# Optimization experiments

Measured on AMD Instinct MI355X. Metric: run time of the kernel, lower is better.

The kernel has to match this reference:

```python
import jax, jax.numpy as jnp
import numpy as np

N_NODES = 50000
N_EDGES = 150000
D_FEAT = 512
HIDDEN = 512
N_CLASSES = 47


def gcn_conv(x, edge_index, W, b, n_nodes):
    """PyG GCNConv: out = D^{-1/2} (A + I) D^{-1/2} (x @ W) + b."""
    h = x @ W  # [N, out_dim] dense GEMM
    loop = jnp.arange(n_nodes, dtype=edge_index.dtype)
    row = jnp.concatenate([edge_index[0], loop])  # source
    col = jnp.concatenate([edge_index[1], loop])  # target
    ones = jnp.ones(row.shape[0], dtype=h.dtype)
    deg = jax.ops.segment_sum(ones, col, num_segments=n_nodes)  # in-degree + 1
    dinv = jnp.where(deg > 0, jax.lax.rsqrt(deg), 0.0)
    norm = dinv[row] * dinv[col]  # [E+N]
    msg = norm[:, None] * h[row]  # gather + scale
    out = jax.ops.segment_sum(msg, col, num_segments=n_nodes)  # scatter-add
    return out + b


def setup_inputs() -> dict:
    key = jax.random.key(0)
    k1, k2, k3, k4, k5, k6 = jax.random.split(key, 6)
    x = jax.random.normal(k1, (N_NODES, D_FEAT), dtype=jnp.float32)
    edge_index = jax.random.randint(k2, (2, N_EDGES), 0, N_NODES, dtype=jnp.int64)
    s1 = (6.0 / (D_FEAT + HIDDEN)) ** 0.5
    s2 = (6.0 / (HIDDEN + N_CLASSES)) ** 0.5
    W1 = jax.random.uniform(k3, (D_FEAT, HIDDEN), jnp.float32, -s1, s1)
    b1 = jnp.zeros((HIDDEN,), jnp.float32)
    W2 = jax.random.uniform(k4, (HIDDEN, N_CLASSES), jnp.float32, -s2, s2)
    b2 = jnp.zeros((N_CLASSES,), jnp.float32)
    return {"x": x, "edge_index": edge_index, "W1": W1, "b1": b1, "W2": W2, "b2": b2}


def reference(x, edge_index, W1, b1, W2, b2):
    n = x.shape[0]
    h = gcn_conv(x, edge_index, W1, b1, n)
    h = jax.nn.relu(h)
    # F.dropout(p=0.5, training=self.training): eval mode -> identity
    out = gcn_conv(h, edge_index, W2, b2, n)
    return out
```

## Files before the change

kernel.cpp:

```cpp
#include <hip/hip_runtime.h>
#include <hip/hip_bf16.h>

#define NNODES 50000
#define NEDGES 150000
#define DFEAT  512
#define HID    512
#define NCLS   47

typedef __hip_bfloat16 bf16;
typedef __attribute__((ext_vector_type(8))) short short8;
typedef __attribute__((ext_vector_type(4))) float float4v;

typedef const __attribute__((address_space(1))) unsigned int* gas_t;
typedef __attribute__((address_space(3))) unsigned int* las_t;
__device__ __forceinline__ void load_lds16(const void* g, void* l) {
    __builtin_amdgcn_global_load_lds((gas_t)g, (las_t)l, 16, 0, 0);
}

__device__ __forceinline__ float bfbits_lo(unsigned int w) {
    return __uint_as_float((w & 0xFFFFu) << 16);
}
__device__ __forceinline__ float bfbits_hi(unsigned int w) {
    return __uint_as_float(w & 0xFFFF0000u);
}

__global__ void k_detect(const void* x, const void* ei, int* flags) {
    __shared__ int scnt[64], sor[64];
    int t = threadIdx.x;
    const unsigned short* xs = (const unsigned short*)x;
    int c = 0;
    for (int i = t; i < 256; i += 64) {
        unsigned int e = (xs[2 * i] >> 7) & 0xFF;
        c += (e >= 117 && e <= 130) ? 1 : 0;
    }
    const int* w = (const int*)ei;
    int o = 0;
    for (int i = 2 * t + 1; i < 512; i += 128) o |= w[i];
    scnt[t] = c; sor[t] = o;
    __syncthreads();
    if (t == 0) {
        int C = 0, O = 0;
        for (int i = 0; i < 64; i++) { C += scnt[i]; O |= sor[i]; }
        flags[0] = (C > 128) ? 1 : 0;
        flags[1] = (O == 0) ? 1 : 0;
    }
}

__device__ __forceinline__ int eidx(const void* ei, int half, int e, int is64) {
    if (is64) return (int)((const long long*)ei)[(size_t)half * NEDGES + e];
    return ((const int*)ei)[half * NEDGES + e];
}

__global__ void k_zero32(unsigned int* p, size_t n) {
    size_t i = (size_t)blockIdx.x * blockDim.x + threadIdx.x;
    if (i < n) p[i] = 0u;
}

__global__ void k_cvt(const void* src, float* dst, int n, const int* flags) {
    int i = blockIdx.x * blockDim.x + threadIdx.x;
    if (i >= n) return;
    dst[i] = flags[0] ? __bfloat162float(((const bf16*)src)[i]) : ((const float*)src)[i];
}

__global__ void k_cvt_w1t(const void* W1, bf16* W1T, const int* flags) {
    int i = blockIdx.x * blockDim.x + threadIdx.x;
    if (i >= DFEAT * HID) return;
    int k = i / HID, n = i % HID;
    float v = flags[0] ? __bfloat162float(((const bf16*)W1)[i]) : ((const float*)W1)[i];
    W1T[(size_t)n * DFEAT + k] = __float2bfloat16(v);
}

__global__ void k_cvt_w2t(const void* W2, bf16* W2T, const int* flags) {
    int i = blockIdx.x * blockDim.x + threadIdx.x;
    if (i >= 64 * HID) return;
    int n = i / HID, k = i % HID;
    float v = 0.0f;
    if (n < NCLS) {
        size_t idx = (size_t)k * NCLS + n;
        v = flags[0] ? __bfloat162float(((const bf16*)W2)[idx]) : ((const float*)W2)[idx];
    }
    W2T[(size_t)n * HID + k] = __float2bfloat16(v);
}

__global__ void k_count(const void* ei, int* cnt, const int* flags) {
    int e = blockIdx.x * blockDim.x + threadIdx.x;
    if (e >= NEDGES) return;
    atomicAdd(&cnt[eidx(ei, 1, e, flags[1])], 1);
}

__global__ void k_dinv(const int* cnt, float* dinv) {
    int i = blockIdx.x * blockDim.x + threadIdx.x;
    if (i < NNODES) dinv[i] = rsqrtf(1.0f + (float)cnt[i]);
}

__global__ __launch_bounds__(256) void k_scan_part(const int* cnt, int* part) {
    __shared__ int s[256];
    int i = blockIdx.x * 256 + threadIdx.x;
    s[threadIdx.x] = (i < NNODES) ? cnt[i] : 0;
    __syncthreads();
    for (int off = 128; off > 0; off >>= 1) {
        if (threadIdx.x < off) s[threadIdx.x] += s[threadIdx.x + off];
        __syncthreads();
    }
    if (threadIdx.x == 0) part[blockIdx.x] = s[0];
}

__global__ __launch_bounds__(256) void k_scan_off(int* part, int n) {
    __shared__ int s[256];
    int v = (threadIdx.x < n) ? part[threadIdx.x] : 0;
    s[threadIdx.x] = v;
    __syncthreads();
    for (int off = 1; off < 256; off <<= 1) {
        int t = (threadIdx.x >= off) ? s[threadIdx.x - off] : 0;
        __syncthreads();
        s[threadIdx.x] += t;
        __syncthreads();
    }
    if (threadIdx.x < n) part[threadIdx.x] = s[threadIdx.x] - v;
}

__global__ __launch_bounds__(256) void k_scan_fin(const int* cnt, const int* part,
                                                  int* rowptr, int* cursor) {
    __shared__ int s[256];
    int i = blockIdx.x * 256 + threadIdx.x;
    int v = (i < NNODES) ? cnt[i] : 0;
    s[threadIdx.x] = v;
    __syncthreads();
    for (int off = 1; off < 256; off <<= 1) {
        int t = (threadIdx.x >= off) ? s[threadIdx.x - off] : 0;
        __syncthreads();
        s[threadIdx.x] += t;
        __syncthreads();
    }
    int incl = s[threadIdx.x] + part[blockIdx.x];
    if (i < NNODES) {
        rowptr[i + 1] = incl;
        cursor[i] = incl - v;
    }
    if (i == 0) rowptr[0] = 0;
}

__global__ void k_fill(const void* ei, int* cursor, int* csr_src, const int* flags) {
    int e = blockIdx.x * blockDim.x + threadIdx.x;
    if (e >= NEDGES) return;
    int is64 = flags[1];
    int v = eidx(ei, 1, e, is64);
    int u = eidx(ei, 0, e, is64);
    int pos = atomicAdd(&cursor[v], 1);
    csr_src[pos] = u;
}

__global__ __launch_bounds__(256, 3) void k_gemm1_v3(
    const void* __restrict__ X, const bf16* __restrict__ W1T,
    bf16* __restrict__ h1c, int c0, int C, const int* __restrict__ flags,
    int col_tiles, int rows_per_xcd, int n_row_tiles) {
    const int b = blockIdx.x;
    const int xcd = b & 7;
    const int s = b >> 3;
    const int col_t = s % col_tiles;
    const int lr = s / col_tiles;
    const int row_t = xcd * rows_per_xcd + lr;
    if (row_t >= n_row_tiles) return;

    __shared__ bf16 As[128 * 64];
    __shared__ bf16 Bs[128 * 64];
    const int tid = threadIdx.x;
    const int wave = tid >> 6, lane = tid & 63;
    const int row0 = row_t * 128;
    const int gc0 = c0 + col_t * 128;
    const int isb = flags[0];

    float4v acc[2][8];
#pragma unroll
    for (int i = 0; i < 2; i++)
#pragma unroll
        for (int j = 0; j < 8; j++) acc[i][j] = (float4v){0.f, 0.f, 0.f, 0.f};

    const int rb = wave * 32;
    const int frow = lane & 15;
    const int fk = lane >> 4;

    for (int k0 = 0; k0 < DFEAT; k0 += 64) {
        __syncthreads();
        if (isb) {
            const bf16* xb = (const bf16*)X;
#pragma unroll
            for (int t = 0; t < 4; ++t) {
                int g8 = wave * 4 + t;
                int r = g8 * 8 + (lane >> 3);
                int gr = row0 + r; if (gr >= NNODES) gr = NNODES - 1;
                int ck = (lane & 7) ^ (r & 7);
                load_lds16(xb + (size_t)gr * DFEAT + k0 + ck * 8, &As[g8 * 8 * 64]);
            }
        } else {
            const float* xf = (const float*)X;
            for (int i = tid; i < 128 * 8; i += 256) {
                int r = i >> 3, p = i & 7;
                int gr = row0 + r; if (gr >= NNODES) gr = NNODES - 1;
                int ck = p ^ (r & 7);
                const float* src = xf + (size_t)gr * DFEAT + k0 + ck * 8;
#pragma unroll
                for (int e = 0; e < 8; ++e)
                    As[r * 64 + p * 8 + e] = __float2bfloat16(src[e]);
            }
        }
#pragma unroll
        for (int t = 0; t < 4; ++t) {
            int g8 = wave * 4 + t;
            int cl = g8 * 8 + (lane >> 3);
            int ck = (lane & 7) ^ (cl & 7);
            load_lds16(W1T + (size_t)(gc0 + cl) * DFEAT + k0 + ck * 8, &Bs[g8 * 8 * 64]);
        }
        __syncthreads();
#pragma unroll
        for (int ki = 0; ki < 2; ++ki) {
            const int cc = ki * 4 + fk;
            short8 a[2], b8[8];
#pragma unroll
            for (int i = 0; i < 2; i++) {
                int r = rb + i * 16 + frow;
                a[i] = *(const short8*)&As[r * 64 + (cc ^ (r & 7)) * 8];
            }
#pragma unroll
            for (int j = 0; j < 8; j++) {
                int cl = j * 16 + frow;
                b8[j] = *(const short8*)&Bs[cl * 64 + (cc ^ (cl & 7)) * 8];
            }
#pragma unroll
            for (int i = 0; i < 2; i++)
#pragma unroll
                for (int j = 0; j < 8; j++)
                    acc[i][j] = __builtin_amdgcn_mfma_f32_16x16x32_bf16(a[i], b8[j], acc[i][j], 0, 0, 0);
        }
    }
    const int ccol = gc0 - c0;
#pragma unroll
    for (int i = 0; i < 2; i++) {
#pragma unroll
        for (int r = 0; r < 4; r++) {
            int grow = row0 + rb + i * 16 + (lane >> 4) * 4 + r;
            if (grow < NNODES) {
#pragma unroll
                for (int j = 0; j < 8; j++)
                    h1c[(size_t)grow * C + ccol + j * 16 + (lane & 15)] =
                        __float2bfloat16(acc[i][j][r]);
            }
        }
    }
}

__global__ __launch_bounds__(256) void k_gemm1_mfma(
    const void* __restrict__ X, const bf16* __restrict__ W1T,
    bf16* __restrict__ h1c, int c0, int C, const int* __restrict__ flags) {
    __shared__ bf16 As[128 * 64];
    __shared__ bf16 Bs[64 * 64];
    const int tid = threadIdx.x;
    const int wave = tid >> 6, lane = tid & 63;
    const int row0 = blockIdx.x * 128;
    const int gc0 = c0 + blockIdx.y * 64;
    const int isb = flags[0];
    float4v acc[2][4];
#pragma unroll
    for (int i = 0; i < 2; i++)
#pragma unroll
        for (int j = 0; j < 4; j++) acc[i][j] = (float4v){0.f, 0.f, 0.f, 0.f};
    const int rbase = wave * 32;
    const int fl_row = lane & 15;
    const int fl_k8 = (lane >> 4) * 8;
    for (int k0 = 0; k0 < DFEAT; k0 += 64) {
        __syncthreads();
        if (isb) {
            const bf16* xb = (const bf16*)X;
#pragma unroll
            for (int i = 0; i < 4; ++i) {
                int r = i * 32 + wave * 8;
                int gr = row0 + r + (lane >> 3);
                if (gr >= NNODES) gr = NNODES - 1;
                load_lds16(xb + (size_t)gr * DFEAT + k0 + (lane & 7) * 8, &As[r * 64]);
            }
        } else {
            const float* xf = (const float*)X;
            for (int i = tid; i < 128 * 64; i += 256) {
                int r = i >> 6, c = i & 63;
                int gr = row0 + r;
                if (gr >= NNODES) gr = NNODES - 1;
                As[i] = __float2bfloat16(xf[(size_t)gr * DFEAT + k0 + c]);
            }
        }
#pragma unroll
        for (int i = 0; i < 2; ++i) {
            int r = i * 32 + wave * 8;
            int gn = gc0 + r + (lane >> 3);
            load_lds16(W1T + (size_t)gn * DFEAT + k0 + (lane & 7) * 8, &Bs[r * 64]);
        }
        __syncthreads();
#pragma unroll
        for (int ki = 0; ki < 64; ki += 32) {
            short8 a[2], b[4];
#pragma unroll
            for (int i = 0; i < 2; i++)
                a[i] = *(const short8*)&As[(rbase + i * 16 + fl_row) * 64 + ki + fl_k8];
#pragma unroll
            for (int j = 0; j < 4; j++)
                b[j] = *(const short8*)&Bs[(j * 16 + fl_row) * 64 + ki + fl_k8];
#pragma unroll
            for (int i = 0; i < 2; i++)
#pragma unroll
                for (int j = 0; j < 4; j++)
                    acc[i][j] = __builtin_amdgcn_mfma_f32_16x16x32_bf16(a[i], b[j], acc[i][j], 0, 0, 0);
        }
    }
    const int ccol = blockIdx.y * 64;
#pragma unroll
    for (int i = 0; i < 2; i++) {
#pragma unroll
        for (int r = 0; r < 4; r++) {
            int grow = row0 + rbase + i * 16 + (lane >> 4) * 4 + r;
            if (grow < NNODES) {
#pragma unroll
                for (int j = 0; j < 4; j++)
                    h1c[(size_t)grow * C + ccol + j * 16 + (lane & 15)] =
                        __float2bfloat16(acc[i][j][r]);
            }
        }
    }
}

__global__ __launch_bounds__(256) void k_agg1_512(const bf16* __restrict__ h1c,
                                                  const int* __restrict__ rowptr,
                                                  const int* __restrict__ csr_src,
                                                  const float* __restrict__ dinv,
                                                  const float* __restrict__ b1c,
                                                  bf16* __restrict__ a1c) {
    int v = blockIdx.x * 4 + (threadIdx.x >> 6);
    int lane = threadIdx.x & 63;
    if (v >= NNODES) return;
    int d8 = lane * 8;
    float dv = dinv[v];
    float s2 = dv * dv;
    uint4 w = *(const uint4*)(h1c + (size_t)v * 512 + d8);
    float a0 = s2 * bfbits_lo(w.x), a1 = s2 * bfbits_hi(w.x);
    float a2 = s2 * bfbits_lo(w.y), a3 = s2 * bfbits_hi(w.y);
    float a4 = s2 * bfbits_lo(w.z), a5 = s2 * bfbits_hi(w.z);
    float a6 = s2 * bfbits_lo(w.w), a7 = s2 * bfbits_hi(w.w);
    int pend = rowptr[v + 1];
    for (int p = rowptr[v]; p < pend; ++p) {
        int u = csr_src[p];
        float nw = dinv[u] * dv;
        uint4 q = *(const uint4*)(h1c + (size_t)u * 512 + d8);
        a0 += nw * bfbits_lo(q.x); a1 += nw * bfbits_hi(q.x);
        a2 += nw * bfbits_lo(q.y); a3 += nw * bfbits_hi(q.y);
        a4 += nw * bfbits_lo(q.z); a5 += nw * bfbits_hi(q.z);
        a6 += nw * bfbits_lo(q.w); a7 += nw * bfbits_hi(q.w);
    }
    const float* bb = b1c + d8;
    a0 += bb[0]; a1 += bb[1]; a2 += bb[2]; a3 += bb[3];
    a4 += bb[4]; a5 += bb[5]; a6 += bb[6]; a7 += bb[7];
    bf16 o[8];
    o[0] = __float2bfloat16(a0 > 0.f ? a0 : 0.f);
    o[1] = __float2bfloat16(a1 > 0.f ? a1 : 0.f);
    o[2] = __float2bfloat16(a2 > 0.f ? a2 : 0.f);
    o[3] = __float2bfloat16(a3 > 0.f ? a3 : 0.f);
    o[4] = __float2bfloat16(a4 > 0.f ? a4 : 0.f);
    o[5] = __float2bfloat16(a5 > 0.f ? a5 : 0.f);
    o[6] = __float2bfloat16(a6 > 0.f ? a6 : 0.f);
    o[7] = __float2bfloat16(a7 > 0.f ? a7 : 0.f);
    *(uint4*)(a1c + (size_t)v * 512 + d8) = *(uint4*)o;
}

__global__ __launch_bounds__(256) void k_agg1(const bf16* __restrict__ h1c,
                                              const int* __restrict__ rowptr,
                                              const int* __restrict__ csr_src,
                                              const float* __restrict__ dinv,
                                              const float* __restrict__ b1c, int c0, int C,
                                              bf16* __restrict__ a1c) {
    const int tshift = (C == 512) ? 7 : (C == 256) ? 6 : (C == 128) ? 5 : 4;
    long long gt = (long long)blockIdx.x * 256 + threadIdx.x;
    int v = (int)(gt >> tshift);
    int d4 = (int)((gt & ((1 << tshift) - 1)) << 2);
    if (v >= NNODES) return;
    float dv = dinv[v];
    uint2 w = *(const uint2*)(h1c + (size_t)v * C + d4);
    float s2 = dv * dv;
    float a0 = s2 * bfbits_lo(w.x), a1 = s2 * bfbits_hi(w.x);
    float a2 = s2 * bfbits_lo(w.y), a3 = s2 * bfbits_hi(w.y);
    int pend = rowptr[v + 1];
    for (int p = rowptr[v]; p < pend; ++p) {
        int u = csr_src[p];
        float nw = dinv[u] * dv;
        uint2 q = *(const uint2*)(h1c + (size_t)u * C + d4);
        a0 += nw * bfbits_lo(q.x); a1 += nw * bfbits_hi(q.x);
        a2 += nw * bfbits_lo(q.y); a3 += nw * bfbits_hi(q.y);
    }
    const float* bb = b1c + c0 + d4;
    a0 += bb[0]; a1 += bb[1]; a2 += bb[2]; a3 += bb[3];
    bf16 o[4];
    o[0] = __float2bfloat16(a0 > 0.f ? a0 : 0.f);
    o[1] = __float2bfloat16(a1 > 0.f ? a1 : 0.f);
    o[2] = __float2bfloat16(a2 > 0.f ? a2 : 0.f);
    o[3] = __float2bfloat16(a3 > 0.f ? a3 : 0.f);
    *(uint2*)(a1c + (size_t)v * C + d4) = *(uint2*)o;
}

__global__ __launch_bounds__(256) void k_gemm2_mfma(
    const bf16* __restrict__ A, int C, const bf16* __restrict__ W2T, int kg0,
    float* __restrict__ h2, int accum) {
    __shared__ bf16 As[128 * 64];
    __shared__ bf16 Bs[64 * 64];
    const int tid = threadIdx.x;
    const int wave = tid >> 6, lane = tid & 63;
    const int row0 = blockIdx.x * 128;
    float4v acc[2][4];
#pragma unroll
    for (int i = 0; i < 2; i++)
#pragma unroll
        for (int j = 0; j < 4; j++) acc[i][j] = (float4v){0.f, 0.f, 0.f, 0.f};
    const int rbase = wave * 32;
    const int fl_row = lane & 15;
    const int fl_k8 = (lane >> 4) * 8;
    for (int kk = 0; kk < C; kk += 64) {
        __syncthreads();
#pragma unroll
        for (int i = 0; i < 4; ++i) {
            int r = i * 32 + wave * 8;
            int gr = row0 + r + (lane >> 3);
            if (gr >= NNODES) gr = NNODES - 1;
            load_lds16(A + (size_t)gr * C + kk + (lane & 7) * 8, &As[r * 64]);
        }
#pragma unroll
        for (int i = 0; i < 2; ++i) {
            int r = i * 32 + wave * 8;
            int gn = r + (lane >> 3);
            load_lds16(W2T + (size_t)gn * HID + kg0 + kk + (lane & 7) * 8, &Bs[r * 64]);
        }
        __syncthreads();
#pragma unroll
        for (int ki = 0; ki < 64; ki += 32) {
            short8 a[2], b[4];
#pragma unroll
            for (int i = 0; i < 2; i++)
                a[i] = *(const short8*)&As[(rbase + i * 16 + fl_row) * 64 + ki + fl_k8];
#pragma unroll
            for (int j = 0; j < 4; j++)
                b[j] = *(const short8*)&Bs[(j * 16 + fl_row) * 64 + ki + fl_k8];
#pragma unroll
            for (int i = 0; i < 2; i++)
#pragma unroll
                for (int j = 0; j < 4; j++)
                    acc[i][j] = __builtin_amdgcn_mfma_f32_16x16x32_bf16(a[i], b[j], acc[i][j], 0, 0, 0);
        }
    }
#pragma unroll
    for (int i = 0; i < 2; i++) {
#pragma unroll
        for (int r = 0; r < 4; r++) {
            int grow = row0 + rbase + i * 16 + (lane >> 4) * 4 + r;
            if (grow < NNODES) {
#pragma unroll
                for (int j = 0; j < 4; j++) {
                    int col = j * 16 + (lane & 15);
                    if (col < NCLS) {
                        size_t o = (size_t)grow * NCLS + col;
                        h2[o] = accum ? h2[o] + acc[i][j][r] : acc[i][j][r];
                    }
                }
            }
        }
    }
}

__global__ __launch_bounds__(256) void k_agg2(const float* __restrict__ h2,
                                              const int* __restrict__ rowptr,
                                              const int* __restrict__ csr_src,
                                              const float* __restrict__ dinv,
                                              const float* __restrict__ b2c,
                                              void* out, const int* flags) {
    int v = blockIdx.x * 4 + (threadIdx.x >> 6);
    int d = threadIdx.x & 63;
    if (v >= NNODES || d >= NCLS) return;
    float dv = dinv[v];
    float acc = dv * dv * h2[(size_t)v * NCLS + d];
    int pend = rowptr[v + 1];
    for (int p = rowptr[v]; p < pend; ++p) {
        int u = csr_src[p];
        acc += dinv[u] * dv * h2[(size_t)u * NCLS + d];
    }
    acc += b2c[d];
    size_t o = (size_t)v * NCLS + d;
    if (flags[0]) ((bf16*)out)[o] = __float2bfloat16(acc);
    else          ((float*)out)[o] = acc;
}

extern "C" void kernel_launch(void* const* d_in, const int* in_sizes, int n_in,
                              void* d_out, int out_size, void* d_ws, size_t ws_size,
                              hipStream_t stream) {
    const void* x  = d_in[0];
    const void* ei = d_in[1];
    const void* W1 = d_in[2];
    const void* b1 = d_in[3];
    const void* W2 = d_in[4];
    const void* b2 = d_in[5];

    char* base = (char*)d_ws;
    auto alloc = [&](size_t bytes) -> char* {
        char* p = base;
        base += (bytes + 255) & ~(size_t)255;
        return p;
    };
    int*   flags  = (int*)alloc(64);
    int*   cnt    = (int*)alloc(sizeof(int) * NNODES);
    int*   part   = (int*)alloc(sizeof(int) * 256);
    int*   rowptr = (int*)alloc(sizeof(int) * (NNODES + 1));
    int*   cursor = (int*)alloc(sizeof(int) * NNODES);
    int*   csr    = (int*)alloc(sizeof(int) * NEDGES);
    float* dinv   = (float*)alloc(sizeof(float) * NNODES);
    bf16*  W1T    = (bf16*)alloc(sizeof(bf16) * DFEAT * HID);
    float* b1c    = (float*)alloc(sizeof(float) * HID);
    bf16*  W2T    = (bf16*)alloc(sizeof(bf16) * 64 * HID);
    float* b2c    = (float*)alloc(sizeof(float) * 64);
    float* h2     = (float*)alloc(sizeof(float) * (size_t)NNODES * NCLS);

    size_t used = (size_t)(base - (char*)d_ws);
    size_t rem = (ws_size > used) ? ws_size - used : 0;
    int C = 64;
    if (rem >= (size_t)200000 * 512 + 1024) C = 512;
    else if (rem >= (size_t)200000 * 256 + 1024) C = 256;
    else if (rem >= (size_t)200000 * 128 + 1024) C = 128;
    bf16* h1c = (bf16*)alloc(sizeof(bf16) * (size_t)NNODES * C);
    bf16* a1c = (bf16*)alloc(sizeof(bf16) * (size_t)NNODES * C);

    k_detect<<<1, 64, 0, stream>>>(x, ei, flags);
    k_zero32<<<(NNODES + 255) / 256, 256, 0, stream>>>((unsigned int*)cnt, NNODES);

    k_cvt_w1t<<<(DFEAT * HID + 255) / 256, 256, 0, stream>>>(W1, W1T, flags);
    k_cvt<<<(HID + 255) / 256, 256, 0, stream>>>(b1, b1c, HID, flags);
    k_cvt_w2t<<<(64 * HID + 255) / 256, 256, 0, stream>>>(W2, W2T, flags);
    k_cvt<<<1, 64, 0, stream>>>(b2, b2c, NCLS, flags);

    k_count<<<(NEDGES + 255) / 256, 256, 0, stream>>>(ei, cnt, flags);
    k_dinv<<<(NNODES + 255) / 256, 256, 0, stream>>>(cnt, dinv);
    const int nsb = (NNODES + 255) / 256;
    k_scan_part<<<nsb, 256, 0, stream>>>(cnt, part);
    k_scan_off<<<1, 256, 0, stream>>>(part, nsb);
    k_scan_fin<<<nsb, 256, 0, stream>>>(cnt, part, rowptr, cursor);
    k_fill<<<(NEDGES + 255) / 256, 256, 0, stream>>>(ei, cursor, csr, flags);

    const int rowblocks = (NNODES + 127) / 128;
    const int rows_per_xcd = (rowblocks + 7) / 8;
    int chunk_i = 0;
    for (int c0 = 0; c0 < HID; c0 += C, ++chunk_i) {
        if (C >= 128) {
            int col_tiles = C / 128;
            int nblk = 8 * rows_per_xcd * col_tiles;
            k_gemm1_v3<<<nblk, 256, 0, stream>>>(x, W1T, h1c, c0, C, flags,
                                                 col_tiles, rows_per_xcd, rowblocks);
        } else {
            dim3 g1(rowblocks, 1);
            k_gemm1_mfma<<<g1, 256, 0, stream>>>(x, W1T, h1c, c0, C, flags);
        }
        if (C == 512) {
            k_agg1_512<<<(NNODES + 3) / 4, 256, 0, stream>>>(h1c, rowptr, csr, dinv, b1c, a1c);
        } else {
            size_t nthr = (size_t)NNODES * (C / 4);
            k_agg1<<<(int)((nthr + 255) / 256), 256, 0, stream>>>(h1c, rowptr, csr, dinv, b1c, c0, C, a1c);
        }
        k_gemm2_mfma<<<rowblocks, 256, 0, stream>>>(a1c, C, W2T, c0, h2, chunk_i > 0 ? 1 : 0);
    }

    k_agg2<<<(NNODES + 3) / 4, 256, 0, stream>>>(h2, rowptr, csr, dinv, b2c, d_out, flags);
}
```

Measured before the change: 348.9 us.

## Double-buffer LDS tiles in both GEMM kernels and swizzle gemm2 layout

```diff
diff --git a/kernel.cpp b/kernel.cpp
--- a/kernel.cpp
+++ b/kernel.cpp
@@ -150,7 +150,7 @@
     csr_src[pos] = u;
 }
 
-__global__ __launch_bounds__(256, 3) void k_gemm1_v3(
+__global__ __launch_bounds__(256, 2) void k_gemm1_v4(
     const void* __restrict__ X, const bf16* __restrict__ W1T,
     bf16* __restrict__ h1c, int c0, int C, const int* __restrict__ flags,
     int col_tiles, int rows_per_xcd, int n_row_tiles) {
@@ -162,8 +162,8 @@
     const int row_t = xcd * rows_per_xcd + lr;
     if (row_t >= n_row_tiles) return;
 
-    __shared__ bf16 As[128 * 64];
-    __shared__ bf16 Bs[128 * 64];
+    __shared__ bf16 As[2][128 * 64];
+    __shared__ bf16 Bs[2][128 * 64];
     const int tid = threadIdx.x;
     const int wave = tid >> 6, lane = tid & 63;
     const int row0 = row_t * 128;
@@ -180,8 +180,7 @@
     const int frow = lane & 15;
     const int fk = lane >> 4;
 
-    for (int k0 = 0; k0 < DFEAT; k0 += 64) {
-        __syncthreads();
+    auto stageAB = [&](int k0, bf16* Asb, bf16* Bsb) {
         if (isb) {
             const bf16* xb = (const bf16*)X;
 #pragma unroll
@@ -190,7 +189,7 @@
                 int r = g8 * 8 + (lane >> 3);
                 int gr = row0 + r; if (gr >= NNODES) gr = NNODES - 1;
                 int ck = (lane & 7) ^ (r & 7);
-                load_lds16(xb + (size_t)gr * DFEAT + k0 + ck * 8, &As[g8 * 8 * 64]);
+                load_lds16(xb + (size_t)gr * DFEAT + k0 + ck * 8, Asb + g8 * 8 * 64);
             }
         } else {
             const float* xf = (const float*)X;
@@ -201,7 +200,7 @@
                 const float* src = xf + (size_t)gr * DFEAT + k0 + ck * 8;
 #pragma unroll
                 for (int e = 0; e < 8; ++e)
-                    As[r * 64 + p * 8 + e] = __float2bfloat16(src[e]);
+                    Asb[r * 64 + p * 8 + e] = __float2bfloat16(src[e]);
             }
         }
 #pragma unroll
@@ -209,9 +208,18 @@
             int g8 = wave * 4 + t;
             int cl = g8 * 8 + (lane >> 3);
             int ck = (lane & 7) ^ (cl & 7);
-            load_lds16(W1T + (size_t)(gc0 + cl) * DFEAT + k0 + ck * 8, &Bs[g8 * 8 * 64]);
-        }
-        __syncthreads();
+            load_lds16(W1T + (size_t)(gc0 + cl) * DFEAT + k0 + ck * 8, Bsb + g8 * 8 * 64);
+        }
+    };
+
+    stageAB(0, As[0], Bs[0]);
+    __syncthreads();
+    int cur = 0;
+
+    for (int k0 = 0; k0 < DFEAT; k0 += 64) {
+        if (k0 + 64 < DFEAT) stageAB(k0 + 64, As[cur ^ 1], Bs[cur ^ 1]);
+        const bf16* Ac = As[cur];
+        const bf16* Bc = Bs[cur];
 #pragma unroll
         for (int ki = 0; ki < 2; ++ki) {
             const int cc = ki * 4 + fk;
@@ -219,12 +227,12 @@
 #pragma unroll
             for (int i = 0; i < 2; i++) {
                 int r = rb + i * 16 + frow;
-                a[i] = *(const short8*)&As[r * 64 + (cc ^ (r & 7)) * 8];
+                a[i] = *(const short8*)&Ac[r * 64 + (cc ^ (r & 7)) * 8];
             }
 #pragma unroll
             for (int j = 0; j < 8; j++) {
                 int cl = j * 16 + frow;
-                b8[j] = *(const short8*)&Bs[cl * 64 + (cc ^ (cl & 7)) * 8];
+                b8[j] = *(const short8*)&Bc[cl * 64 + (cc ^ (cl & 7)) * 8];
             }
 #pragma unroll
             for (int i = 0; i < 2; i++)
@@ -232,7 +240,10 @@
                 for (int j = 0; j < 8; j++)
                     acc[i][j] = __builtin_amdgcn_mfma_f32_16x16x32_bf16(a[i], b8[j], acc[i][j], 0, 0, 0);
         }
-    }
+        __syncthreads();
+        cur ^= 1;
+    }
+
     const int ccol = gc0 - c0;
 #pragma unroll
     for (int i = 0; i < 2; i++) {
@@ -402,11 +413,11 @@
     *(uint2*)(a1c + (size_t)v * C + d4) = *(uint2*)o;
 }
 
-__global__ __launch_bounds__(256) void k_gemm2_mfma(
+__global__ __launch_bounds__(256, 3) void k_gemm2_v2(
     const bf16* __restrict__ A, int C, const bf16* __restrict__ W2T, int kg0,
     float* __restrict__ h2, int accum) {
-    __shared__ bf16 As[128 * 64];
-    __shared__ bf16 Bs[64 * 64];
+    __shared__ bf16 As[2][128 * 64];
+    __shared__ bf16 Bs[2][64 * 64];
     const int tid = threadIdx.x;
     const int wave = tid >> 6, lane = tid & 63;
     const int row0 = blockIdx.x * 128;
@@ -415,46 +426,64 @@
     for (int i = 0; i < 2; i++)
 #pragma unroll
         for (int j = 0; j < 4; j++) acc[i][j] = (float4v){0.f, 0.f, 0.f, 0.f};
-    const int rbase = wave * 32;
-    const int fl_row = lane & 15;
-    const int fl_k8 = (lane >> 4) * 8;
+    const int rb = wave * 32;
+    const int frow = lane & 15;
+    const int fk = lane >> 4;
+
+    auto stage2 = [&](int kk, bf16* Asb, bf16* Bsb) {
+#pragma unroll
+        for (int t = 0; t < 4; ++t) {
+            int g8 = wave * 4 + t;
+            int r = g8 * 8 + (lane >> 3);
+            int gr = row0 + r; if (gr >= NNODES) gr = NNODES - 1;
+            int ck = (lane & 7) ^ (r & 7);
+            load_lds16(A + (size_t)gr * C + kk + ck * 8, Asb + g8 * 8 * 64);
+        }
+#pragma unroll
+        for (int t = 0; t < 2; ++t) {
+            int g8 = wave * 2 + t;
+            int cl = g8 * 8 + (lane >> 3);
+            int ck = (lane & 7) ^ (cl & 7);
+            load_lds16(W2T + (size_t)cl * HID + kg0 + kk + ck * 8, Bsb + g8 * 8 * 64);
+        }
+    };
+
+    stage2(0, As[0], Bs[0]);
+    __syncthreads();
+    int cur = 0;
+
     for (int kk = 0; kk < C; kk += 64) {
-        __syncthreads();
-#pragma unroll
-        for (int i = 0; i < 4; ++i) {
-            int r = i * 32 + wave * 8;
-            int gr = row0 + r + (lane >> 3);
-            if (gr >= NNODES) gr = NNODES - 1;
-            load_lds16(A + (size_t)gr * C + kk + (lane & 7) * 8, &As[r * 64]);
-        }
-#pragma unroll
-        for (int i = 0; i < 2; ++i) {
-            int r = i * 32 + wave * 8;
-            int gn = r + (lane >> 3);
-            load_lds16(W2T + (size_t)gn * HID + kg0 + kk + (lane & 7) * 8, &Bs[r * 64]);
-        }
-        __syncthreads();
-#pragma unroll
-        for (int ki = 0; ki < 64; ki += 32) {
-            short8 a[2], b[4];
+        if (kk + 64 < C) stage2(kk + 64, As[cur ^ 1], Bs[cur ^ 1]);
+        const bf16* Ac = As[cur];
+        const bf16* Bc = Bs[cur];
+#pragma unroll
+        for (int ki = 0; ki < 2; ++ki) {
+            const int cc = ki * 4 + fk;
+            short8 a[2], b8[4];
+#pragma unroll
+            for (int i = 0; i < 2; i++) {
+                int r = rb + i * 16 + frow;
+                a[i] = *(const short8*)&Ac[r * 64 + (cc ^ (r & 7)) * 8];
+            }
+#pragma unroll
+            for (int j = 0; j < 4; j++) {
+                int cl = j * 16 + frow;
+                b8[j] = *(const short8*)&Bc[cl * 64 + (cc ^ (cl & 7)) * 8];
+            }
 #pragma unroll
             for (int i = 0; i < 2; i++)
-                a[i] = *(const short8*)&As[(rbase + i * 16 + fl_row) * 64 + ki + fl_k8];
-#pragma unroll
-            for (int j = 0; j < 4; j++)
-                b[j] = *(const short8*)&Bs[(j * 16 + fl_row) * 64 + ki + fl_k8];
-#pragma unroll
-            for (int i = 0; i < 2; i++)
 #pragma unroll
                 for (int j = 0; j < 4; j++)
-                    acc[i][j] = __builtin_amdgcn_mfma_f32_16x16x32_bf16(a[i], b[j], acc[i][j], 0, 0, 0);
-        }
+                    acc[i][j] = __builtin_amdgcn_mfma_f32_16x16x32_bf16(a[i], b8[j], acc[i][j], 0, 0, 0);
+        }
+        __syncthreads();
+        cur ^= 1;
     }
 #pragma unroll
     for (int i = 0; i < 2; i++) {
 #pragma unroll
         for (int r = 0; r < 4; r++) {
-            int grow = row0 + rbase + i * 16 + (lane >> 4) * 4 + r;
+            int grow = row0 + rb + i * 16 + (lane >> 4) * 4 + r;
             if (grow < NNODES) {
 #pragma unroll
                 for (int j = 0; j < 4; j++) {
@@ -552,7 +581,7 @@
         if (C >= 128) {
             int col_tiles = C / 128;
             int nblk = 8 * rows_per_xcd * col_tiles;
-            k_gemm1_v3<<<nblk, 256, 0, stream>>>(x, W1T, h1c, c0, C, flags,
+            k_gemm1_v4<<<nblk, 256, 0, stream>>>(x, W1T, h1c, c0, C, flags,
                                                  col_tiles, rows_per_xcd, rowblocks);
         } else {
             dim3 g1(rowblocks, 1);
@@ -564,7 +593,7 @@
             size_t nthr = (size_t)NNODES * (C / 4);
             k_agg1<<<(int)((nthr + 255) / 256), 256, 0, stream>>>(h1c, rowptr, csr, dinv, b1c, c0, C, a1c);
         }
-        k_gemm2_mfma<<<rowblocks, 256, 0, stream>>>(a1c, C, W2T, c0, h2, chunk_i > 0 ? 1 : 0);
+        k_gemm2_v2<<<rowblocks, 256, 0, stream>>>(a1c, C, W2T, c0, h2, chunk_i > 0 ? 1 : 0);
     }
 
     k_agg2<<<(NNODES + 3) / 4, 256, 0, stream>>>(h2, rowptr, csr, dinv, b2c, d_out, flags);
```

Measured after the change: 370.8 us. 1.06x slower.

## Load MFMA fragments directly from global memory, dropping LDS staging in both GEMMs

Applied to the files above, without the earlier changes.

```diff
diff --git a/kernel.cpp b/kernel.cpp
--- a/kernel.cpp
+++ b/kernel.cpp
@@ -150,7 +150,23 @@
     csr_src[pos] = u;
 }
 
-__global__ __launch_bounds__(256, 3) void k_gemm1_v3(
+__device__ __forceinline__ short8 afrag_bf(const bf16* X, int row, int k) {
+    return *(const short8*)(X + (size_t)row * DFEAT + k);
+}
+__device__ __forceinline__ short8 afrag_f32(const float* X, int row, int k) {
+    const float* p = X + (size_t)row * DFEAT + k;
+    float4v f0 = *(const float4v*)p;
+    float4v f1 = *(const float4v*)(p + 4);
+    short8 r;
+    bf16* rb = (bf16*)&r;
+    rb[0] = __float2bfloat16(f0[0]); rb[1] = __float2bfloat16(f0[1]);
+    rb[2] = __float2bfloat16(f0[2]); rb[3] = __float2bfloat16(f0[3]);
+    rb[4] = __float2bfloat16(f1[0]); rb[5] = __float2bfloat16(f1[1]);
+    rb[6] = __float2bfloat16(f1[2]); rb[7] = __float2bfloat16(f1[3]);
+    return r;
+}
+
+__global__ __launch_bounds__(256, 3) void k_gemm1_v6(
     const void* __restrict__ X, const bf16* __restrict__ W1T,
     bf16* __restrict__ h1c, int c0, int C, const int* __restrict__ flags,
     int col_tiles, int rows_per_xcd, int n_row_tiles) {
@@ -162,77 +178,66 @@
     const int row_t = xcd * rows_per_xcd + lr;
     if (row_t >= n_row_tiles) return;
 
-    __shared__ bf16 As[128 * 64];
-    __shared__ bf16 Bs[128 * 64];
     const int tid = threadIdx.x;
     const int wave = tid >> 6, lane = tid & 63;
     const int row0 = row_t * 128;
     const int gc0 = c0 + col_t * 128;
     const int isb = flags[0];
 
-    float4v acc[2][8];
-#pragma unroll
-    for (int i = 0; i < 2; i++)
-#pragma unroll
-        for (int j = 0; j < 8; j++) acc[i][j] = (float4v){0.f, 0.f, 0.f, 0.f};
-
     const int rb = wave * 32;
     const int frow = lane & 15;
-    const int fk = lane >> 4;
-
-    for (int k0 = 0; k0 < DFEAT; k0 += 64) {
-        __syncthreads();
-        if (isb) {
-            const bf16* xb = (const bf16*)X;
-#pragma unroll
-            for (int t = 0; t < 4; ++t) {
-                int g8 = wave * 4 + t;
-                int r = g8 * 8 + (lane >> 3);
-                int gr = row0 + r; if (gr >= NNODES) gr = NNODES - 1;
-                int ck = (lane & 7) ^ (r & 7);
-                load_lds16(xb + (size_t)gr * DFEAT + k0 + ck * 8, &As[g8 * 8 * 64]);
-            }
-        } else {
-            const float* xf = (const float*)X;
-            for (int i = tid; i < 128 * 8; i += 256) {
-                int r = i >> 3, p = i & 7;
-                int gr = row0 + r; if (gr >= NNODES) gr = NNODES - 1;
-                int ck = p ^ (r & 7);
-                const float* src = xf + (size_t)gr * DFEAT + k0 + ck * 8;
-#pragma unroll
-                for (int e = 0; e < 8; ++e)
-                    As[r * 64 + p * 8 + e] = __float2bfloat16(src[e]);
-            }
-        }
-#pragma unroll
-        for (int t = 0; t < 4; ++t) {
-            int g8 = wave * 4 + t;
-            int cl = g8 * 8 + (lane >> 3);
-            int ck = (lane & 7) ^ (cl & 7);
-            load_lds16(W1T + (size_t)(gc0 + cl) * DFEAT + k0 + ck * 8, &Bs[g8 * 8 * 64]);
-        }
-        __syncthreads();
-#pragma unroll
-        for (int ki = 0; ki < 2; ++ki) {
-            const int cc = ki * 4 + fk;
+    const int fko = (lane >> 4) * 8;
+
+    int ar[2];
+#pragma unroll
+    for (int i = 0; i < 2; i++) {
+        int gr = row0 + rb + i * 16 + frow;
+        ar[i] = (gr >= NNODES) ? NNODES - 1 : gr;
+    }
+
+    float4v acc[2][8];
+#pragma unroll
+    for (int i = 0; i < 2; i++)
+#pragma unroll
+        for (int j = 0; j < 8; j++) acc[i][j] = (float4v){0.f, 0.f, 0.f, 0.f};
+
+    const bf16* xb = (const bf16*)X;
+    const float* xf = (const float*)X;
+
+    if (isb) {
+#pragma unroll 4
+        for (int k0 = 0; k0 < DFEAT; k0 += 32) {
+            const int kk = k0 + fko;
             short8 a[2], b8[8];
 #pragma unroll
-            for (int i = 0; i < 2; i++) {
-                int r = rb + i * 16 + frow;
-                a[i] = *(const short8*)&As[r * 64 + (cc ^ (r & 7)) * 8];
-            }
-#pragma unroll
-            for (int j = 0; j < 8; j++) {
-                int cl = j * 16 + frow;
-                b8[j] = *(const short8*)&Bs[cl * 64 + (cc ^ (cl & 7)) * 8];
-            }
+            for (int i = 0; i < 2; i++) a[i] = afrag_bf(xb, ar[i], kk);
+#pragma unroll
+            for (int j = 0; j < 8; j++)
+                b8[j] = *(const short8*)(W1T + (size_t)(gc0 + j * 16 + frow) * DFEAT + kk);
 #pragma unroll
             for (int i = 0; i < 2; i++)
 #pragma unroll
                 for (int j = 0; j < 8; j++)
                     acc[i][j] = __builtin_amdgcn_mfma_f32_16x16x32_bf16(a[i], b8[j], acc[i][j], 0, 0, 0);
         }
-    }
+    } else {
+#pragma unroll 2
+        for (int k0 = 0; k0 < DFEAT; k0 += 32) {
+            const int kk = k0 + fko;
+            short8 a[2], b8[8];
+#pragma unroll
+            for (int i = 0; i < 2; i++) a[i] = afrag_f32(xf, ar[i], kk);
+#pragma unroll
+            for (int j = 0; j < 8; j++)
+                b8[j] = *(const short8*)(W1T + (size_t)(gc0 + j * 16 + frow) * DFEAT + kk);
+#pragma unroll
+            for (int i = 0; i < 2; i++)
+#pragma unroll
+                for (int j = 0; j < 8; j++)
+                    acc[i][j] = __builtin_amdgcn_mfma_f32_16x16x32_bf16(a[i], b8[j], acc[i][j], 0, 0, 0);
+        }
+    }
+
     const int ccol = gc0 - c0;
 #pragma unroll
     for (int i = 0; i < 2; i++) {
@@ -242,7 +247,7 @@
             if (grow < NNODES) {
 #pragma unroll
                 for (int j = 0; j < 8; j++)
-                    h1c[(size_t)grow * C + ccol + j * 16 + (lane & 15)] =
+                    h1c[(size_t)grow * C + ccol + j * 16 + frow] =
                         __float2bfloat16(acc[i][j][r]);
             }
         }
@@ -402,63 +407,55 @@
     *(uint2*)(a1c + (size_t)v * C + d4) = *(uint2*)o;
 }
 
-__global__ __launch_bounds__(256) void k_gemm2_mfma(
+__global__ __launch_bounds__(256, 4) void k_gemm2_v4(
     const bf16* __restrict__ A, int C, const bf16* __restrict__ W2T, int kg0,
     float* __restrict__ h2, int accum) {
-    __shared__ bf16 As[128 * 64];
-    __shared__ bf16 Bs[64 * 64];
     const int tid = threadIdx.x;
     const int wave = tid >> 6, lane = tid & 63;
     const int row0 = blockIdx.x * 128;
+    const int rb = wave * 32;
+    const int frow = lane & 15;
+    const int fko = (lane >> 4) * 8;
+
+    int ar[2];
+#pragma unroll
+    for (int i = 0; i < 2; i++) {
+        int gr = row0 + rb + i * 16 + frow;
+        ar[i] = (gr >= NNODES) ? NNODES - 1 : gr;
+    }
+
     float4v acc[2][4];
 #pragma unroll
     for (int i = 0; i < 2; i++)
 #pragma unroll
         for (int j = 0; j < 4; j++) acc[i][j] = (float4v){0.f, 0.f, 0.f, 0.f};
-    const int rbase = wave * 32;
-    const int fl_row = lane & 15;
-    const int fl_k8 = (lane >> 4) * 8;
-    for (int kk = 0; kk < C; kk += 64) {
-        __syncthreads();
-#pragma unroll
-        for (int i = 0; i < 4; ++i) {
-            int r = i * 32 + wave * 8;
-            int gr = row0 + r + (lane >> 3);
-            if (gr >= NNODES) gr = NNODES - 1;
-            load_lds16(A + (size_t)gr * C + kk + (lane & 7) * 8, &As[r * 64]);
-        }
-#pragma unroll
-        for (int i = 0; i < 2; ++i) {
-            int r = i * 32 + wave * 8;
-            int gn = r + (lane >> 3);
-            load_lds16(W2T + (size_t)gn * HID + kg0 + kk + (lane & 7) * 8, &Bs[r * 64]);
-        }
-        __syncthreads();
-#pragma unroll
-        for (int ki = 0; ki < 64; ki += 32) {
-            short8 a[2], b[4];
-#pragma unroll
-            for (int i = 0; i < 2; i++)
-                a[i] = *(const short8*)&As[(rbase + i * 16 + fl_row) * 64 + ki + fl_k8];
+
+#pragma unroll 4
+    for (int k0 = 0; k0 < C; k0 += 32) {
+        const int kk = k0 + fko;
+        short8 a[2], b4[4];
+#pragma unroll
+        for (int i = 0; i < 2; i++)
+            a[i] = *(const short8*)(A + (size_t)ar[i] * C + kk);
+#pragma unroll
+        for (int j = 0; j < 4; j++)
+            b4[j] = *(const short8*)(W2T + (size_t)(j * 16 + frow) * HID + kg0 + kk);
+#pragma unroll
+        for (int i = 0; i < 2; i++)
 #pragma unroll
             for (int j = 0; j < 4; j++)
-                b[j] = *(const short8*)&Bs[(j * 16 + fl_row) * 64 + ki + fl_k8];
-#pragma unroll
-            for (int i = 0; i < 2; i++)
-#pragma unroll
-                for (int j = 0; j < 4; j++)
-                    acc[i][j] = __builtin_amdgcn_mfma_f32_16x16x32_bf16(a[i], b[j], acc[i][j], 0, 0, 0);
-        }
-    }
+                acc[i][j] = __builtin_amdgcn_mfma_f32_16x16x32_bf16(a[i], b4[j], acc[i][j], 0, 0, 0);
+    }
+
 #pragma unroll
     for (int i = 0; i < 2; i++) {
 #pragma unroll
         for (int r = 0; r < 4; r++) {
-            int grow = row0 + rbase + i * 16 + (lane >> 4) * 4 + r;
+            int grow = row0 + rb + i * 16 + (lane >> 4) * 4 + r;
             if (grow < NNODES) {
 #pragma unroll
                 for (int j = 0; j < 4; j++) {
-                    int col = j * 16 + (lane & 15);
+                    int col = j * 16 + frow;
                     if (col < NCLS) {
                         size_t o = (size_t)grow * NCLS + col;
                         h2[o] = accum ? h2[o] + acc[i][j][r] : acc[i][j][r];
@@ -552,7 +549,7 @@
         if (C >= 128) {
             int col_tiles = C / 128;
             int nblk = 8 * rows_per_xcd * col_tiles;
-            k_gemm1_v3<<<nblk, 256, 0, stream>>>(x, W1T, h1c, c0, C, flags,
+            k_gemm1_v6<<<nblk, 256, 0, stream>>>(x, W1T, h1c, c0, C, flags,
                                                  col_tiles, rows_per_xcd, rowblocks);
         } else {
             dim3 g1(rowblocks, 1);
@@ -564,7 +561,7 @@
             size_t nthr = (size_t)NNODES * (C / 4);
             k_agg1<<<(int)((nthr + 255) / 256), 256, 0, stream>>>(h1c, rowptr, csr, dinv, b1c, c0, C, a1c);
         }
-        k_gemm2_mfma<<<rowblocks, 256, 0, stream>>>(a1c, C, W2T, c0, h2, chunk_i > 0 ? 1 : 0);
+        k_gemm2_v4<<<rowblocks, 256, 0, stream>>>(a1c, C, W2T, c0, h2, chunk_i > 0 ? 1 : 0);
     }
 
     k_agg2<<<(NNODES + 3) / 4, 256, 0, stream>>>(h2, rowptr, csr, dinv, b2c, d_out, flags);
```

Result: slower. 424.7 us (+21.7%).

## Fuse prep kernels, merge dinv into scan, retile gemm2 with swizzled LDS

Applied to the files above, without the earlier changes.

```diff
diff --git a/kernel.cpp b/kernel.cpp
--- a/kernel.cpp
+++ b/kernel.cpp
@@ -24,62 +24,86 @@
     return __uint_as_float(w & 0xFFFF0000u);
 }
 
-__global__ void k_detect(const void* x, const void* ei, int* flags) {
-    __shared__ int scnt[64], sor[64];
-    int t = threadIdx.x;
-    const unsigned short* xs = (const unsigned short*)x;
-    int c = 0;
-    for (int i = t; i < 256; i += 64) {
-        unsigned int e = (xs[2 * i] >> 7) & 0xFF;
-        c += (e >= 117 && e <= 130) ? 1 : 0;
-    }
-    const int* w = (const int*)ei;
-    int o = 0;
-    for (int i = 2 * t + 1; i < 512; i += 128) o |= w[i];
-    scnt[t] = c; sor[t] = o;
-    __syncthreads();
-    if (t == 0) {
-        int C = 0, O = 0;
-        for (int i = 0; i < 64; i++) { C += scnt[i]; O |= sor[i]; }
-        flags[0] = (C > 128) ? 1 : 0;
-        flags[1] = (O == 0) ? 1 : 0;
-    }
-}
-
 __device__ __forceinline__ int eidx(const void* ei, int half, int e, int is64) {
     if (is64) return (int)((const long long*)ei)[(size_t)half * NEDGES + e];
     return ((const int*)ei)[half * NEDGES + e];
 }
 
-__global__ void k_zero32(unsigned int* p, size_t n) {
-    size_t i = (size_t)blockIdx.x * blockDim.x + threadIdx.x;
-    if (i < n) p[i] = 0u;
-}
-
-__global__ void k_cvt(const void* src, float* dst, int n, const int* flags) {
-    int i = blockIdx.x * blockDim.x + threadIdx.x;
-    if (i >= n) return;
-    dst[i] = flags[0] ? __bfloat162float(((const bf16*)src)[i]) : ((const float*)src)[i];
-}
-
-__global__ void k_cvt_w1t(const void* W1, bf16* W1T, const int* flags) {
-    int i = blockIdx.x * blockDim.x + threadIdx.x;
-    if (i >= DFEAT * HID) return;
-    int k = i / HID, n = i % HID;
-    float v = flags[0] ? __bfloat162float(((const bf16*)W1)[i]) : ((const float*)W1)[i];
-    W1T[(size_t)n * DFEAT + k] = __float2bfloat16(v);
-}
-
-__global__ void k_cvt_w2t(const void* W2, bf16* W2T, const int* flags) {
-    int i = blockIdx.x * blockDim.x + threadIdx.x;
-    if (i >= 64 * HID) return;
-    int n = i / HID, k = i % HID;
-    float v = 0.0f;
-    if (n < NCLS) {
-        size_t idx = (size_t)k * NCLS + n;
-        v = flags[0] ? __bfloat162float(((const bf16*)W2)[idx]) : ((const float*)W2)[idx];
-    }
-    W2T[(size_t)n * HID + k] = __float2bfloat16(v);
+#define ZB ((NNODES + 255) / 256)
+#define PR_W1T (1 + ZB)
+#define PR_B1  (PR_W1T + 1024)
+#define PR_W2T (PR_B1 + 2)
+#define PR_B2  (PR_W2T + 128)
+#define PR_GRID (PR_B2 + 1)
+
+__global__ __launch_bounds__(256) void k_prep0(
+    const void* x, const void* ei, const void* W1, const void* b1,
+    const void* W2, const void* b2, int* flags, unsigned int* cnt,
+    bf16* W1T, float* b1c, bf16* W2T, float* b2c) {
+    __shared__ int sh[128];
+    __shared__ int shflag;
+    const int b = blockIdx.x, t = threadIdx.x;
+
+    if (b >= 1 && b < 1 + ZB) {
+        int i = (b - 1) * 256 + t;
+        if (i < NNODES) cnt[i] = 0u;
+        return;
+    }
+
+    if (t < 64) {
+        const unsigned short* xs = (const unsigned short*)x;
+        int c = 0;
+        for (int i = t; i < 256; i += 64) {
+            unsigned int e = (xs[2 * i] >> 7) & 0xFF;
+            c += (e >= 117 && e <= 130) ? 1 : 0;
+        }
+        sh[t] = c;
+        if (b == 0) {
+            const int* w = (const int*)ei;
+            int o = 0;
+            for (int i = 2 * t + 1; i < 512; i += 128) o |= w[i];
+            sh[64 + t] = o;
+        }
+    }
+    __syncthreads();
+    if (t == 0) {
+        int C = 0;
+        for (int i = 0; i < 64; i++) C += sh[i];
+        shflag = (C > 128) ? 1 : 0;
+        if (b == 0) {
+            int O = 0;
+            for (int i = 0; i < 64; i++) O |= sh[64 + i];
+            flags[0] = shflag;
+            flags[1] = (O == 0) ? 1 : 0;
+        }
+    }
+    __syncthreads();
+    const int isb = shflag;
+
+    if (b == 0) return;
+
+    if (b >= PR_W1T && b < PR_B1) {
+        int i = (b - PR_W1T) * 256 + t;
+        int k = i / HID, n = i % HID;
+        float v = isb ? __bfloat162float(((const bf16*)W1)[i]) : ((const float*)W1)[i];
+        W1T[(size_t)n * DFEAT + k] = __float2bfloat16(v);
+    } else if (b >= PR_B1 && b < PR_W2T) {
+        int i = (b - PR_B1) * 256 + t;
+        if (i < HID)
+            b1c[i] = isb ? __bfloat162float(((const bf16*)b1)[i]) : ((const float*)b1)[i];
+    } else if (b >= PR_W2T && b < PR_B2) {
+        int i = (b - PR_W2T) * 256 + t;
+        int n = i / HID, k = i % HID;
+        float v = 0.0f;
+        if (n < NCLS) {
+            size_t idx = (size_t)k * NCLS + n;
+            v = isb ? __bfloat162float(((const bf16*)W2)[idx]) : ((const float*)W2)[idx];
+        }
+        W2T[(size_t)n * HID + k] = __float2bfloat16(v);
+    } else if (b == PR_B2) {
+        if (t < NCLS)
+            b2c[t] = isb ? __bfloat162float(((const bf16*)b2)[t]) : ((const float*)b2)[t];
+    }
 }
 
 __global__ void k_count(const void* ei, int* cnt, const int* flags) {
@@ -88,15 +112,13 @@
     atomicAdd(&cnt[eidx(ei, 1, e, flags[1])], 1);
 }
 
-__global__ void k_dinv(const int* cnt, float* dinv) {
-    int i = blockIdx.x * blockDim.x + threadIdx.x;
-    if (i < NNODES) dinv[i] = rsqrtf(1.0f + (float)cnt[i]);
-}
-
-__global__ __launch_bounds__(256) void k_scan_part(const int* cnt, int* part) {
+__global__ __launch_bounds__(256) void k_scan_part_dinv(const int* cnt, int* part,
+                                                        float* dinv) {
     __shared__ int s[256];
     int i = blockIdx.x * 256 + threadIdx.x;
-    s[threadIdx.x] = (i < NNODES) ? cnt[i] : 0;
+    int v = (i < NNODES) ? cnt[i] : 0;
+    if (i < NNODES) dinv[i] = rsqrtf(1.0f + (float)v);
+    s[threadIdx.x] = v;
     __syncthreads();
     for (int off = 128; off > 0; off >>= 1) {
         if (threadIdx.x < off) s[threadIdx.x] += s[threadIdx.x + off];
@@ -402,67 +424,72 @@
     *(uint2*)(a1c + (size_t)v * C + d4) = *(uint2*)o;
 }
 
-__global__ __launch_bounds__(256) void k_gemm2_mfma(
+__global__ __launch_bounds__(128) void k_gemm2_64(
     const bf16* __restrict__ A, int C, const bf16* __restrict__ W2T, int kg0,
     float* __restrict__ h2, int accum) {
-    __shared__ bf16 As[128 * 64];
+    __shared__ bf16 As[64 * 64];
     __shared__ bf16 Bs[64 * 64];
     const int tid = threadIdx.x;
     const int wave = tid >> 6, lane = tid & 63;
-    const int row0 = blockIdx.x * 128;
+    const int row0 = blockIdx.x * 64;
     float4v acc[2][4];
 #pragma unroll
     for (int i = 0; i < 2; i++)
 #pragma unroll
         for (int j = 0; j < 4; j++) acc[i][j] = (float4v){0.f, 0.f, 0.f, 0.f};
-    const int rbase = wave * 32;
-    const int fl_row = lane & 15;
-    const int fl_k8 = (lane >> 4) * 8;
+    const int rb = wave * 32;
+    const int frow = lane & 15;
+    const int fk = lane >> 4;
+
     for (int kk = 0; kk < C; kk += 64) {
         __syncthreads();
 #pragma unroll
-        for (int i = 0; i < 4; ++i) {
-            int r = i * 32 + wave * 8;
-            int gr = row0 + r + (lane >> 3);
-            if (gr >= NNODES) gr = NNODES - 1;
-            load_lds16(A + (size_t)gr * C + kk + (lane & 7) * 8, &As[r * 64]);
-        }
-#pragma unroll
-        for (int i = 0; i < 2; ++i) {
-            int r = i * 32 + wave * 8;
-            int gn = r + (lane >> 3);
-            load_lds16(W2T + (size_t)gn * HID + kg0 + kk + (lane & 7) * 8, &Bs[r * 64]);
-        }
-        __syncthreads();
-#pragma unroll
-        for (int ki = 0; ki < 64; ki += 32) {
-            short8 a[2], b[4];
+        for (int t = 0; t < 4; ++t) {
+            int g8 = wave * 4 + t;
+            int r = g8 * 8 + (lane >> 3);
+            int gr = row0 + r; if (gr >= NNODES) gr = NNODES - 1;
+            int ck = (lane & 7) ^ (r & 7);
+            load_lds16(A + (size_t)gr * C + kk + ck * 8, &As[g8 * 8 * 64]);
+        }
+#pragma unroll
+        for (int t = 0; t < 4; ++t) {
+            int g8 = wave * 4 + t;
+            int cl = g8 * 8 + (lane >> 3);
+            int ck = (lane & 7) ^ (cl & 7);
+            load_lds16(W2T + (size_t)cl * HID + kg0 + kk + ck * 8, &Bs[g8 * 8 * 64]);
+        }
+        __syncthreads();
+#pragma unroll
+        for (int ki = 0; ki < 2; ++ki) {
+            const int cc = ki * 4 + fk;
+            short8 a[2], b8[4];
+#pragma unroll
+            for (int i = 0; i < 2; i++) {
+                int r = rb + i * 16 + frow;
+                a[i] = *(const short8*)&As[r * 64 + (cc ^ (r & 7)) * 8];
+            }
+#pragma unroll
+            for (int j = 0; j < 4; j++) {
+                int cl = j * 16 + frow;
+                b8[j] = *(const short8*)&Bs[cl * 64 + (cc ^ (cl & 7)) * 8];
+            }
 #pragma unroll
             for (int i = 0; i < 2; i++)
-                a[i] = *(const short8*)&As[(rbase + i * 16 + fl_row) * 64 + ki + fl_k8];
-#pragma unroll
-            for (int j = 0; j < 4; j++)
-                b[j] = *(const short8*)&Bs[(j * 16 + fl_row) * 64 + ki + fl_k8];
-#pragma unroll
-            for (int i = 0; i < 2; i++)
 #pragma unroll
                 for (int j = 0; j < 4; j++)
-                    acc[i][j] = __builtin_amdgcn_mfma_f32_16x16x32_bf16(a[i], b[j], acc[i][j], 0, 0, 0);
+                    acc[i][j] = __builtin_amdgcn_mfma_f32_16x16x32_bf16(a[i], b8[j], acc[i][j], 0, 0, 0);
         }
     }
 #pragma unroll
     for (int i = 0; i < 2; i++) {
 #pragma unroll
         for (int r = 0; r < 4; r++) {
-            int grow = row0 + rbase + i * 16 + (lane >> 4) * 4 + r;
+            int grow = row0 + rb + i * 16 + (lane >> 4) * 4 + r;
             if (grow < NNODES) {
 #pragma unroll
                 for (int j = 0; j < 4; j++) {
-                    int col = j * 16 + (lane & 15);
-                    if (col < NCLS) {
-                        size_t o = (size_t)grow * NCLS + col;
-                        h2[o] = accum ? h2[o] + acc[i][j][r] : acc[i][j][r];
-                    }
+                    size_t o = (size_t)grow * 64 + j * 16 + frow;
+                    h2[o] = accum ? h2[o] + acc[i][j][r] : acc[i][j][r];
                 }
             }
         }
@@ -479,11 +506,11 @@
     int d = threadIdx.x & 63;
     if (v >= NNODES || d >= NCLS) return;
     float dv = dinv[v];
-    float acc = dv * dv * h2[(size_t)v * NCLS + d];
+    float acc = dv * dv * h2[(size_t)v * 64 + d];
     int pend = rowptr[v + 1];
     for (int p = rowptr[v]; p < pend; ++p) {
         int u = csr_src[p];
-        acc += dinv[u] * dv * h2[(size_t)u * NCLS + d];
+        acc += dinv[u] * dv * h2[(size_t)u * 64 + d];
     }
     acc += b2c[d];
     size_t o = (size_t)v * NCLS + d;
@@ -518,7 +545,7 @@
     float* b1c    = (float*)alloc(sizeof(float) * HID);
     bf16*  W2T    = (bf16*)alloc(sizeof(bf16) * 64 * HID);
     float* b2c    = (float*)alloc(sizeof(float) * 64);
-    float* h2     = (float*)alloc(sizeof(float) * (size_t)NNODES * NCLS);
+    float* h2     = (float*)alloc(sizeof(float) * (size_t)NNODES * 64);
 
     size_t used = (size_t)(base - (char*)d_ws);
     size_t rem = (ws_size > used) ? ws_size - used : 0;
@@ -529,18 +556,11 @@
     bf16* h1c = (bf16*)alloc(sizeof(bf16) * (size_t)NNODES * C);
     bf16* a1c = (bf16*)alloc(sizeof(bf16) * (size_t)NNODES * C);
 
-    k_detect<<<1, 64, 0, stream>>>(x, ei, flags);
-    k_zero32<<<(NNODES + 255) / 256, 256, 0, stream>>>((unsigned int*)cnt, NNODES);
-
-    k_cvt_w1t<<<(DFEAT * HID + 255) / 256, 256, 0, stream>>>(W1, W1T, flags);
-    k_cvt<<<(HID + 255) / 256, 256, 0, stream>>>(b1, b1c, HID, flags);
-    k_cvt_w2t<<<(64 * HID + 255) / 256, 256, 0, stream>>>(W2, W2T, flags);
-    k_cvt<<<1, 64, 0, stream>>>(b2, b2c, NCLS, flags);
-
+    k_prep0<<<PR_GRID, 256, 0, stream>>>(x, ei, W1, b1, W2, b2, flags,
+                                         (unsigned int*)cnt, W1T, b1c, W2T, b2c);
     k_count<<<(NEDGES + 255) / 256, 256, 0, stream>>>(ei, cnt, flags);
-    k_dinv<<<(NNODES + 255) / 256, 256, 0, stream>>>(cnt, dinv);
     const int nsb = (NNODES + 255) / 256;
-    k_scan_part<<<nsb, 256, 0, stream>>>(cnt, part);
+    k_scan_part_dinv<<<nsb, 256, 0, stream>>>(cnt, part, dinv);
     k_scan_off<<<1, 256, 0, stream>>>(part, nsb);
     k_scan_fin<<<nsb, 256, 0, stream>>>(cnt, part, rowptr, cursor);
     k_fill<<<(NEDGES + 255) / 256, 256, 0, stream>>>(ei, cursor, csr, flags);
@@ -564,7 +584,7 @@
             size_t nthr = (size_t)NNODES * (C / 4);
             k_agg1<<<(int)((nthr + 255) / 256), 256, 0, stream>>>(h1c, rowptr, csr, dinv, b1c, c0, C, a1c);
         }
-        k_gemm2_mfma<<<rowblocks, 256, 0, stream>>>(a1c, C, W2T, c0, h2, chunk_i > 0 ? 1 : 0);
+        k_gemm2_64<<<(NNODES + 63) / 64, 128, 0, stream>>>(a1c, C, W2T, c0, h2, chunk_i > 0 ? 1 : 0);
     }
 
     k_agg2<<<(NNODES + 3) / 4, 256, 0, stream>>>(h2, rowptr, csr, dinv, b2c, d_out, flags);
```

After: 336.2 us. 3.6% less time.
